# Kernel tuning notes

Measured on AMD Instinct MI355X. Metric: run time of the kernel, lower is better.

## Reference

```python
import jax, jax.numpy as jnp
import numpy as np

D = 1024
H = 16
DK = D // H


def apply_rope(x):
    # x: [B, H, T, dk]; interleaved-pair RoPE as in the torch source
    T, dim = x.shape[-2], x.shape[-1]
    inv_freq = 1.0 / (10000.0 ** (jnp.arange(0, dim, 2, dtype=x.dtype) / dim))  # [dk/2]
    pos = jnp.arange(T, dtype=x.dtype)
    sinusoid = pos[:, None] * inv_freq[None, :]  # [T, dk/2]
    sin, cos = jnp.sin(sinusoid), jnp.cos(sinusoid)
    x1, x2 = x[..., ::2], x[..., 1::2]
    rot = jnp.stack([x1 * cos - x2 * sin, x1 * sin + x2 * cos], axis=-1)
    return rot.reshape(x.shape)


def setup_inputs() -> dict:
    key = jax.random.key(0)
    k1, k2, k3, k4, k5 = jax.random.split(key, 5)
    B, T = 2, 2048
    s = 1.0 / np.sqrt(D)
    return {
        "x": jax.random.normal(k1, (B, T, D), dtype=jnp.float32),
        "W_qkv": jax.random.normal(k2, (D, 3 * D), dtype=jnp.float32) * s,
        "b_qkv": jnp.zeros((3 * D,), dtype=jnp.float32),
        "W_out": jax.random.normal(k3, (D, D), dtype=jnp.float32) * s,
        "b_out": jnp.zeros((D,), dtype=jnp.float32),
    }


def reference(x, W_qkv, b_qkv, W_out, b_out):
    B, T, C = x.shape
    qkv = x @ W_qkv + b_qkv  # [B, T, 3D]
    qkv = qkv.reshape(B, T, 3, H, DK).transpose(2, 0, 3, 1, 4)  # [3, B, H, T, dk]
    q, k, v = qkv[0], qkv[1], qkv[2]
    q, k = apply_rope(q), apply_rope(k)
    scores = jnp.einsum("bhtd,bhsd->bhts", q, k) / jnp.sqrt(jnp.asarray(DK, x.dtype))
    causal = jnp.tril(jnp.ones((T, T), dtype=bool))
    scores = jnp.where(causal, scores, jnp.asarray(-1e9, x.dtype))
    probs = jax.nn.softmax(scores, axis=-1)
    attn = jnp.einsum("bhts,bhsd->bhtd", probs, v)  # [B, H, T, dk]
    out = attn.transpose(0, 2, 1, 3).reshape(B, T, C)  # b h t d -> b t (h d)
    return out @ W_out + b_out
```

## Files before the change

### kernel.cpp

```cpp
#include <hip/hip_runtime.h>
#include <math.h>

#define DMODEL 1024
#define NHEAD  16
#define HDK    64
#define BATCH  2
#define SEQ    2048
#define MROWS  (BATCH*SEQ)
#define NQKV   (3*DMODEL)
#define LOG2_10000 13.287712379549449f
#define INV2PI 0.15915494309189535f
#define SCALE_LOG2E 0.1803368801111137f
#define M_FIX 8.0f

typedef __attribute__((ext_vector_type(8))) short bf16x8;
typedef __attribute__((ext_vector_type(4))) float f32x4;

__device__ __forceinline__ short f2bf(float f) {
    union { float f; unsigned u; } v; v.f = f;
    unsigned r = v.u + 0x7fffu + ((v.u >> 16) & 1u);
    return (short)(r >> 16);
}

__device__ __forceinline__ short bf_hi(float f) {
    union { float f; unsigned u; } v; v.f = f;
    return (short)(v.u >> 16);
}

__device__ __forceinline__ float fast_exp2(float x) {
#if __has_builtin(__builtin_amdgcn_exp2f)
    return __builtin_amdgcn_exp2f(x);
#else
    return exp2f(x);
#endif
}

__device__ __forceinline__ void gld_lds16(const short* g, short* l) {
    __builtin_amdgcn_global_load_lds(
        (const __attribute__((address_space(1))) void*)g,
        (__attribute__((address_space(3))) void*)l, 16, 0, 0);
}

__global__ __launch_bounds__(256) void prep_kernel(
    const float* __restrict__ x, const float* __restrict__ wqkv,
    const float* __restrict__ wout,
    short* __restrict__ xb, short* __restrict__ wqkv_t, short* __restrict__ wout_t)
{
    __shared__ short tile[32][33];
    const int tid = threadIdx.x;
    if (blockIdx.x < 2048) {
        const int i = (blockIdx.x * 256 + tid) * 8;
        float4 a = *(const float4*)(x + i);
        float4 b = *(const float4*)(x + i + 4);
        bf16x8 o;
        o[0] = f2bf(a.x); o[1] = f2bf(a.y); o[2] = f2bf(a.z); o[3] = f2bf(a.w);
        o[4] = f2bf(b.x); o[5] = f2bf(b.y); o[6] = f2bf(b.z); o[7] = f2bf(b.w);
        *(bf16x8*)(xb + i) = o;
        return;
    }
    const int bx = blockIdx.x - 2048;
    int nx = bx & 127;
    const int ky = bx >> 7;
    const float* in; short* out; int N;
    if (nx < 96) { in = wqkv; out = wqkv_t; N = NQKV; }
    else         { in = wout; out = wout_t; N = DMODEL; nx -= 96; }
    const int tx = tid & 31, ty = tid >> 5;
    const int n0 = nx * 32, k0 = ky * 32;
    #pragma unroll
    for (int i = 0; i < 32; i += 8)
        tile[ty + i][tx] = f2bf(in[(size_t)(k0 + ty + i) * N + n0 + tx]);
    __syncthreads();
    #pragma unroll
    for (int i = 0; i < 32; i += 8)
        out[(size_t)(n0 + ty + i) * DMODEL + k0 + tx] = tile[tx][ty + i];
}

__global__ __launch_bounds__(256) void qkv_gemm_kernel(
    const short* __restrict__ xb, const short* __restrict__ Wt,
    const float* __restrict__ bias,
    short* __restrict__ qd, short* __restrict__ kd, short* __restrict__ vtb)
{
    __shared__ __align__(16) short As[128 * 32];
    __shared__ __align__(16) short Bs[128 * 32];
    const int tid = threadIdx.x;
    const int lane = tid & 63, wave = tid >> 6;
    const int wm = wave & 1, wn = wave >> 1;
    const int l15 = lane & 15, quad = lane >> 4;
    const int n0 = blockIdx.x * 128, m0 = blockIdx.y * 128;
    const int srow = lane >> 2, sc = lane & 3;

    const short* gA1 = xb + (size_t)(m0 + wave * 32 + srow) * DMODEL + sc * 8;
    const short* gA2 = gA1 + (size_t)16 * DMODEL;
    const short* gB1 = Wt + (size_t)(n0 + wave * 32 + srow) * DMODEL + sc * 8;
    const short* gB2 = gB1 + (size_t)16 * DMODEL;
    short* lA1 = As + (wave * 32) * 32;
    short* lA2 = As + (wave * 32 + 16) * 32;
    short* lB1 = Bs + (wave * 32) * 32;
    short* lB2 = Bs + (wave * 32 + 16) * 32;

    f32x4 zero = {0.f, 0.f, 0.f, 0.f};
    f32x4 acc[4][4];
    #pragma unroll
    for (int i = 0; i < 4; ++i)
        #pragma unroll
        for (int j = 0; j < 4; ++j) acc[i][j] = zero;

    for (int k0 = 0; k0 < DMODEL; k0 += 32) {
        __syncthreads();
        gld_lds16(gA1 + k0, lA1);
        gld_lds16(gA2 + k0, lA2);
        gld_lds16(gB1 + k0, lB1);
        gld_lds16(gB2 + k0, lB2);
        __syncthreads();
        bf16x8 af[4], bfr[4];
        #pragma unroll
        for (int i = 0; i < 4; ++i)
            af[i] = *(const bf16x8*)&As[(wm * 64 + i * 16 + l15) * 32 + quad * 8];
        #pragma unroll
        for (int j = 0; j < 4; ++j)
            bfr[j] = *(const bf16x8*)&Bs[(wn * 64 + j * 16 + l15) * 32 + quad * 8];
        #pragma unroll
        for (int i = 0; i < 4; ++i)
            #pragma unroll
            for (int j = 0; j < 4; ++j)
                acc[i][j] = __builtin_amdgcn_mfma_f32_16x16x32_bf16(af[i], bfr[j], acc[i][j], 0, 0, 0);
    }

    const int which = n0 >> 10;
    float biasv[4], invf[4];
    int hh[4], dd[4];
    #pragma unroll
    for (int j = 0; j < 4; ++j) {
        const int n = n0 + wn * 64 + j * 16 + l15;
        biasv[j] = bias[n];
        hh[j] = (n & 1023) >> 6;
        dd[j] = n & 63;
        invf[j] = INV2PI * exp2f(-((float)(dd[j] & ~1) / 64.f) * LOG2_10000);
    }
    #pragma unroll
    for (int i = 0; i < 4; ++i) {
        #pragma unroll
        for (int r = 0; r < 4; ++r) {
            const int m = m0 + wm * 64 + i * 16 + quad * 4 + r;
            const int b = m >> 11, t = m & (SEQ - 1);
            #pragma unroll
            for (int j = 0; j < 4; ++j) {
                float val = acc[i][j][r] + biasv[j];
                if (which < 2) {
                    const float rev = (float)t * invf[j];
                    const float fr = rev - floorf(rev);
                    const float s = __builtin_amdgcn_sinf(fr);
                    const float c = __builtin_amdgcn_cosf(fr);
                    const float partner = __shfl_xor(val, 1);
                    val = (lane & 1) ? (partner * s + val * c) : (val * c - partner * s);
                    short* dst = (which == 0) ? qd : kd;
                    dst[((size_t)(b * NHEAD + hh[j]) * SEQ + t) * HDK + dd[j]] = f2bf(val);
                } else {
                    vtb[((size_t)(b * NHEAD + hh[j]) * HDK + dd[j]) * SEQ + t] = f2bf(val);
                }
            }
        }
    }
}

__global__ __launch_bounds__(256) void attn_mfma_kernel(
    const short* __restrict__ qd, const short* __restrict__ kd,
    const short* __restrict__ vt, short* __restrict__ od)
{
    __shared__ __align__(16) short Ks[2][2][64 * 32];
    __shared__ __align__(16) short Vs[2][2][64 * 32];
    __shared__ __align__(16) short Ps[4][16][66];
    const int tid = threadIdx.x, lane = tid & 63, w = tid >> 6;
    const int l15 = lane & 15, quad = lane >> 4;
    const int id = (int)blockIdx.x;
    const int c = id & 7, kk = id >> 3;
    const int qp = kk & 15, jj = kk >> 4;
    const int hb = c + 8 * jj;
    const int h = hb & 15, b = hb >> 4;
    const size_t base = ((size_t)(b * NHEAD + h)) * SEQ * HDK;
    const int srow = tid >> 2, sc = tid & 3;
    const int lofs = tid * 8;
    f32x4 zero = {0.f, 0.f, 0.f, 0.f};

    const int qtile[2] = { qp, 31 - qp };
    const short* kp0 = kd + base + (size_t)srow * HDK + sc * 8;
    const short* vp0 = vt + base + (size_t)srow * SEQ + sc * 8;
    const short* kp1 = kp0 + (size_t)64 * HDK;
    const short* vp1 = vp0 + 64;

    #pragma unroll 1
    for (int qi = 0; qi < 2; ++qi) {
        const int q0 = qtile[qi] * 64;
        bf16x8 qf[2];
        {
            const short* qrow = qd + base + (size_t)(q0 + w * 16 + l15) * HDK;
            qf[0] = *(const bf16x8*)(qrow + quad * 8);
            qf[1] = *(const bf16x8*)(qrow + 32 + quad * 8);
        }
        float l_acc[4] = {0.f, 0.f, 0.f, 0.f};
        f32x4 o[4];
        #pragma unroll
        for (int j = 0; j < 4; ++j) o[j] = zero;

        const int nkt = q0 / 64 + 1;
        const int npair = (nkt + 1) >> 1;

        bf16x8 rk[2][2], rv[2][2];
        rk[0][0] = *(const bf16x8*)kp0; rk[0][1] = *(const bf16x8*)(kp0 + 32);
        rv[0][0] = *(const bf16x8*)vp0; rv[0][1] = *(const bf16x8*)(vp0 + 32);
        rk[1][0] = *(const bf16x8*)kp1; rk[1][1] = *(const bf16x8*)(kp1 + 32);
        rv[1][0] = *(const bf16x8*)vp1; rv[1][1] = *(const bf16x8*)(vp1 + 32);

        for (int p = 0; p < npair; ++p) {
            __syncthreads();
            *(bf16x8*)&Ks[0][0][lofs] = rk[0][0]; *(bf16x8*)&Ks[0][1][lofs] = rk[0][1];
            *(bf16x8*)&Vs[0][0][lofs] = rv[0][0]; *(bf16x8*)&Vs[0][1][lofs] = rv[0][1];
            *(bf16x8*)&Ks[1][0][lofs] = rk[1][0]; *(bf16x8*)&Ks[1][1][lofs] = rk[1][1];
            *(bf16x8*)&Vs[1][0][lofs] = rv[1][0]; *(bf16x8*)&Vs[1][1][lofs] = rv[1][1];
            __syncthreads();
            if (p + 1 < npair) {
                const int sn = (2 * p + 2) * 64;
                const short* kn = kd + base + (size_t)(sn + srow) * HDK + sc * 8;
                const short* vn = vt + base + (size_t)srow * SEQ + sn + sc * 8;
                rk[0][0] = *(const bf16x8*)kn; rk[0][1] = *(const bf16x8*)(kn + 32);
                rv[0][0] = *(const bf16x8*)vn; rv[0][1] = *(const bf16x8*)(vn + 32);
                const short* kn2 = kn + (size_t)64 * HDK;
                const short* vn2 = vn + 64;
                rk[1][0] = *(const bf16x8*)kn2; rk[1][1] = *(const bf16x8*)(kn2 + 32);
                rv[1][0] = *(const bf16x8*)vn2; rv[1][1] = *(const bf16x8*)(vn2 + 32);
            } else if (qi == 0) {
                rk[0][0] = *(const bf16x8*)kp0; rk[0][1] = *(const bf16x8*)(kp0 + 32);
                rv[0][0] = *(const bf16x8*)vp0; rv[0][1] = *(const bf16x8*)(vp0 + 32);
                rk[1][0] = *(const bf16x8*)kp1; rk[1][1] = *(const bf16x8*)(kp1 + 32);
                rv[1][0] = *(const bf16x8*)vp1; rv[1][1] = *(const bf16x8*)(vp1 + 32);
            }

            #pragma unroll
            for (int tt = 0; tt < 2; ++tt) {
                const int kt = 2 * p + tt;
                if (tt == 1 && kt >= nkt) break;
                f32x4 sacc[4];
                #pragma unroll
                for (int j = 0; j < 4; ++j) {
                    bf16x8 kf0 = *(const bf16x8*)&Ks[tt][0][(j * 16 + l15) * 32 + quad * 8];
                    bf16x8 kf1 = *(const bf16x8*)&Ks[tt][1][(j * 16 + l15) * 32 + quad * 8];
                    sacc[j] = __builtin_amdgcn_mfma_f32_16x16x32_bf16(qf[0], kf0, zero, 0, 0, 0);
                    sacc[j] = __builtin_amdgcn_mfma_f32_16x16x32_bf16(qf[1], kf1, sacc[j], 0, 0, 0);
                }
                if (kt == nkt - 1) {
                    const int s0 = kt * 64;
                    #pragma unroll
                    for (int j = 0; j < 4; ++j) {
                        const int scol = s0 + j * 16 + l15;
                        #pragma unroll
                        for (int r = 0; r < 4; ++r) {
                            const int trow = q0 + w * 16 + quad * 4 + r;
                            const float sv = sacc[j][r] * SCALE_LOG2E - M_FIX;
                            const float pv = (scol > trow) ? 0.f : fast_exp2(sv);
                            l_acc[r] += pv;
                            Ps[w][quad * 4 + r][j * 16 + l15] = bf_hi(pv);
                        }
                    }
                } else {
                    #pragma unroll
                    for (int j = 0; j < 4; ++j)
                        #pragma unroll
                        for (int r = 0; r < 4; ++r) {
                            const float pv = fast_exp2(sacc[j][r] * SCALE_LOG2E - M_FIX);
                            l_acc[r] += pv;
                            Ps[w][quad * 4 + r][j * 16 + l15] = bf_hi(pv);
                        }
                }
                bf16x8 pf0 = *(const bf16x8*)&Ps[w][l15][quad * 8];
                bf16x8 pf1 = *(const bf16x8*)&Ps[w][l15][32 + quad * 8];
                #pragma unroll
                for (int j = 0; j < 4; ++j) {
                    bf16x8 vf0 = *(const bf16x8*)&Vs[tt][0][(j * 16 + l15) * 32 + quad * 8];
                    bf16x8 vf1 = *(const bf16x8*)&Vs[tt][1][(j * 16 + l15) * 32 + quad * 8];
                    o[j] = __builtin_amdgcn_mfma_f32_16x16x32_bf16(pf0, vf0, o[j], 0, 0, 0);
                    o[j] = __builtin_amdgcn_mfma_f32_16x16x32_bf16(pf1, vf1, o[j], 0, 0, 0);
                }
            }
        }

        #pragma unroll
        for (int r = 0; r < 4; ++r) {
            float sr = l_acc[r];
            #pragma unroll
            for (int off = 1; off < 16; off <<= 1) sr += __shfl_xor(sr, off);
            l_acc[r] = sr;
        }
        #pragma unroll
        for (int r = 0; r < 4; ++r) {
            const float inv = 1.f / l_acc[r];
            const int t = q0 + w * 16 + quad * 4 + r;
            #pragma unroll
            for (int j = 0; j < 4; ++j)
                od[((size_t)(b * SEQ + t) * NHEAD + h) * HDK + j * 16 + l15] =
                    f2bf(o[j][r] * inv);
        }
    }
}

__global__ __launch_bounds__(256) void out_gemm_kernel(
    const short* __restrict__ Ab, const short* __restrict__ Wt,
    const float* __restrict__ bias, float* __restrict__ out)
{
    __shared__ __align__(16) short As[128 * 32];
    __shared__ __align__(16) short Bs[128 * 32];
    const int tid = threadIdx.x;
    const int lane = tid & 63, wave = tid >> 6;
    const int wm = wave & 1, wn = wave >> 1;
    const int l15 = lane & 15, quad = lane >> 4;
    const int n0 = blockIdx.x * 128, m0 = blockIdx.y * 128;
    const int srow = lane >> 2, sc = lane & 3;

    const short* gA1 = Ab + (size_t)(m0 + wave * 32 + srow) * DMODEL + sc * 8;
    const short* gA2 = gA1 + (size_t)16 * DMODEL;
    const short* gB1 = Wt + (size_t)(n0 + wave * 32 + srow) * DMODEL + sc * 8;
    const short* gB2 = gB1 + (size_t)16 * DMODEL;
    short* lA1 = As + (wave * 32) * 32;
    short* lA2 = As + (wave * 32 + 16) * 32;
    short* lB1 = Bs + (wave * 32) * 32;
    short* lB2 = Bs + (wave * 32 + 16) * 32;

    f32x4 zero = {0.f, 0.f, 0.f, 0.f};
    f32x4 acc[4][4];
    #pragma unroll
    for (int i = 0; i < 4; ++i)
        #pragma unroll
        for (int j = 0; j < 4; ++j) acc[i][j] = zero;

    for (int k0 = 0; k0 < DMODEL; k0 += 32) {
        __syncthreads();
        gld_lds16(gA1 + k0, lA1);
        gld_lds16(gA2 + k0, lA2);
        gld_lds16(gB1 + k0, lB1);
        gld_lds16(gB2 + k0, lB2);
        __syncthreads();
        bf16x8 af[4], bfr[4];
        #pragma unroll
        for (int i = 0; i < 4; ++i)
            af[i] = *(const bf16x8*)&As[(wm * 64 + i * 16 + l15) * 32 + quad * 8];
        #pragma unroll
        for (int j = 0; j < 4; ++j)
            bfr[j] = *(const bf16x8*)&Bs[(wn * 64 + j * 16 + l15) * 32 + quad * 8];
        #pragma unroll
        for (int i = 0; i < 4; ++i)
            #pragma unroll
            for (int j = 0; j < 4; ++j)
                acc[i][j] = __builtin_amdgcn_mfma_f32_16x16x32_bf16(af[i], bfr[j], acc[i][j], 0, 0, 0);
    }

    #pragma unroll
    for (int j = 0; j < 4; ++j) {
        const int n = n0 + wn * 64 + j * 16 + l15;
        const float bv = bias[n];
        #pragma unroll
        for (int i = 0; i < 4; ++i)
            #pragma unroll
            for (int r = 0; r < 4; ++r) {
                const int m = m0 + wm * 64 + i * 16 + quad * 4 + r;
                out[(size_t)m * DMODEL + n] = acc[i][j][r] + bv;
            }
    }
}

extern "C" void kernel_launch(void* const* d_in, const int* in_sizes, int n_in,
                              void* d_out, int out_size, void* d_ws, size_t ws_size,
                              hipStream_t stream) {
    const float* x    = (const float*)d_in[0];
    const float* Wqkv = (const float*)d_in[1];
    const float* bqkv = (const float*)d_in[2];
    const float* Wout = (const float*)d_in[3];
    const float* bout = (const float*)d_in[4];
    float* out = (float*)d_out;

    short* ws = (short*)d_ws;
    short* xb     = ws;
    short* wqkv_t = xb + (size_t)4 * 1024 * 1024;
    short* wout_t = wqkv_t + (size_t)3 * 1024 * 1024;
    short* qd     = wout_t + (size_t)1024 * 1024;
    short* kd     = qd + (size_t)4 * 1024 * 1024;
    short* vtb    = kd + (size_t)4 * 1024 * 1024;
    short* attn   = vtb + (size_t)4 * 1024 * 1024;

    prep_kernel<<<2048 + 4096, 256, 0, stream>>>(x, Wqkv, Wout, xb, wqkv_t, wout_t);

    qkv_gemm_kernel<<<dim3(NQKV / 128, MROWS / 128), 256, 0, stream>>>(
        xb, wqkv_t, bqkv, qd, kd, vtb);

    attn_mfma_kernel<<<512, 256, 0, stream>>>(qd, kd, vtb, attn);

    out_gemm_kernel<<<dim3(DMODEL / 128, MROWS / 128), 256, 0, stream>>>(
        attn, wout_t, bout, out);
}
```

Baseline: 198.3 us.

## Process paired causal query tiles jointly, sharing each K/V tile load

Each block used to run its two query tiles (qp and 31-qp) one after the other, loading the key/value tiles twice. Now both tiles are processed in one pass over the key tiles, so every staged K/V tile feeds both query tiles while the short tile is still active. Global and LDS traffic for K/V drops and the work per barrier grows. In exchange the wave holds more live registers (two accumulator sets), K/V staging drops from two tiles per iteration to one so there are more barriers, and the extra register pressure may lower occupancy.

```diff
diff --git a/kernel.cpp b/kernel.cpp
--- a/kernel.cpp
+++ b/kernel.cpp
@@ -167,9 +167,9 @@
     const short* __restrict__ qd, const short* __restrict__ kd,
     const short* __restrict__ vt, short* __restrict__ od)
 {
-    __shared__ __align__(16) short Ks[2][2][64 * 32];
-    __shared__ __align__(16) short Vs[2][2][64 * 32];
-    __shared__ __align__(16) short Ps[4][16][66];
+    __shared__ __align__(16) short Ks[2][64 * 32];
+    __shared__ __align__(16) short Vs[2][64 * 32];
+    __shared__ __align__(16) short Ps[4][2][16][66];
     const int tid = threadIdx.x, lane = tid & 63, w = tid >> 6;
     const int l15 = lane & 15, quad = lane >> 4;
     const int id = (int)blockIdx.x;
@@ -182,122 +182,152 @@
     const int lofs = tid * 8;
     f32x4 zero = {0.f, 0.f, 0.f, 0.f};
 
-    const int qtile[2] = { qp, 31 - qp };
-    const short* kp0 = kd + base + (size_t)srow * HDK + sc * 8;
-    const short* vp0 = vt + base + (size_t)srow * SEQ + sc * 8;
-    const short* kp1 = kp0 + (size_t)64 * HDK;
-    const short* vp1 = vp0 + 64;
-
-    #pragma unroll 1
-    for (int qi = 0; qi < 2; ++qi) {
-        const int q0 = qtile[qi] * 64;
-        bf16x8 qf[2];
-        {
-            const short* qrow = qd + base + (size_t)(q0 + w * 16 + l15) * HDK;
-            qf[0] = *(const bf16x8*)(qrow + quad * 8);
-            qf[1] = *(const bf16x8*)(qrow + 32 + quad * 8);
-        }
-        float l_acc[4] = {0.f, 0.f, 0.f, 0.f};
-        f32x4 o[4];
-        #pragma unroll
-        for (int j = 0; j < 4; ++j) o[j] = zero;
-
-        const int nkt = q0 / 64 + 1;
-        const int npair = (nkt + 1) >> 1;
-
-        bf16x8 rk[2][2], rv[2][2];
-        rk[0][0] = *(const bf16x8*)kp0; rk[0][1] = *(const bf16x8*)(kp0 + 32);
-        rv[0][0] = *(const bf16x8*)vp0; rv[0][1] = *(const bf16x8*)(vp0 + 32);
-        rk[1][0] = *(const bf16x8*)kp1; rk[1][1] = *(const bf16x8*)(kp1 + 32);
-        rv[1][0] = *(const bf16x8*)vp1; rv[1][1] = *(const bf16x8*)(vp1 + 32);
-
-        for (int p = 0; p < npair; ++p) {
-            __syncthreads();
-            *(bf16x8*)&Ks[0][0][lofs] = rk[0][0]; *(bf16x8*)&Ks[0][1][lofs] = rk[0][1];
-            *(bf16x8*)&Vs[0][0][lofs] = rv[0][0]; *(bf16x8*)&Vs[0][1][lofs] = rv[0][1];
-            *(bf16x8*)&Ks[1][0][lofs] = rk[1][0]; *(bf16x8*)&Ks[1][1][lofs] = rk[1][1];
-            *(bf16x8*)&Vs[1][0][lofs] = rv[1][0]; *(bf16x8*)&Vs[1][1][lofs] = rv[1][1];
-            __syncthreads();
-            if (p + 1 < npair) {
-                const int sn = (2 * p + 2) * 64;
-                const short* kn = kd + base + (size_t)(sn + srow) * HDK + sc * 8;
-                const short* vn = vt + base + (size_t)srow * SEQ + sn + sc * 8;
-                rk[0][0] = *(const bf16x8*)kn; rk[0][1] = *(const bf16x8*)(kn + 32);
-                rv[0][0] = *(const bf16x8*)vn; rv[0][1] = *(const bf16x8*)(vn + 32);
-                const short* kn2 = kn + (size_t)64 * HDK;
-                const short* vn2 = vn + 64;
-                rk[1][0] = *(const bf16x8*)kn2; rk[1][1] = *(const bf16x8*)(kn2 + 32);
-                rv[1][0] = *(const bf16x8*)vn2; rv[1][1] = *(const bf16x8*)(vn2 + 32);
-            } else if (qi == 0) {
-                rk[0][0] = *(const bf16x8*)kp0; rk[0][1] = *(const bf16x8*)(kp0 + 32);
-                rv[0][0] = *(const bf16x8*)vp0; rv[0][1] = *(const bf16x8*)(vp0 + 32);
-                rk[1][0] = *(const bf16x8*)kp1; rk[1][1] = *(const bf16x8*)(kp1 + 32);
-                rv[1][0] = *(const bf16x8*)vp1; rv[1][1] = *(const bf16x8*)(vp1 + 32);
-            }
-
-            #pragma unroll
-            for (int tt = 0; tt < 2; ++tt) {
-                const int kt = 2 * p + tt;
-                if (tt == 1 && kt >= nkt) break;
-                f32x4 sacc[4];
+    const int q0A = qp * 64;
+    const int q0B = (31 - qp) * 64;
+    const int nktB = 32 - qp;
+
+    bf16x8 qfA[2], qfB[2];
+    {
+        const short* qrA = qd + base + (size_t)(q0A + w * 16 + l15) * HDK;
+        qfA[0] = *(const bf16x8*)(qrA + quad * 8);
+        qfA[1] = *(const bf16x8*)(qrA + 32 + quad * 8);
+        const short* qrB = qd + base + (size_t)(q0B + w * 16 + l15) * HDK;
+        qfB[0] = *(const bf16x8*)(qrB + quad * 8);
+        qfB[1] = *(const bf16x8*)(qrB + 32 + quad * 8);
+    }
+    float lA[4] = {0.f, 0.f, 0.f, 0.f}, lB[4] = {0.f, 0.f, 0.f, 0.f};
+    f32x4 oA[4], oB[4];
+    #pragma unroll
+    for (int j = 0; j < 4; ++j) { oA[j] = zero; oB[j] = zero; }
+
+    const short* kp = kd + base + (size_t)srow * HDK + sc * 8;
+    const short* vp = vt + base + (size_t)srow * SEQ + sc * 8;
+    bf16x8 rk0 = *(const bf16x8*)kp, rk1 = *(const bf16x8*)(kp + 32);
+    bf16x8 rv0 = *(const bf16x8*)vp, rv1 = *(const bf16x8*)(vp + 32);
+
+    for (int kt = 0; kt < nktB; ++kt) {
+        __syncthreads();
+        *(bf16x8*)&Ks[0][lofs] = rk0; *(bf16x8*)&Ks[1][lofs] = rk1;
+        *(bf16x8*)&Vs[0][lofs] = rv0; *(bf16x8*)&Vs[1][lofs] = rv1;
+        __syncthreads();
+        if (kt + 1 < nktB) {
+            const short* kn = kp + (size_t)(kt + 1) * 64 * HDK;
+            const short* vn = vp + (kt + 1) * 64;
+            rk0 = *(const bf16x8*)kn; rk1 = *(const bf16x8*)(kn + 32);
+            rv0 = *(const bf16x8*)vn; rv1 = *(const bf16x8*)(vn + 32);
+        }
+        const bool doA = (kt <= qp);
+
+        f32x4 sA[4], sB[4];
+        #pragma unroll
+        for (int j = 0; j < 4; ++j) {
+            bf16x8 kf0 = *(const bf16x8*)&Ks[0][(j * 16 + l15) * 32 + quad * 8];
+            bf16x8 kf1 = *(const bf16x8*)&Ks[1][(j * 16 + l15) * 32 + quad * 8];
+            sB[j] = __builtin_amdgcn_mfma_f32_16x16x32_bf16(qfB[0], kf0, zero, 0, 0, 0);
+            sB[j] = __builtin_amdgcn_mfma_f32_16x16x32_bf16(qfB[1], kf1, sB[j], 0, 0, 0);
+            if (doA) {
+                sA[j] = __builtin_amdgcn_mfma_f32_16x16x32_bf16(qfA[0], kf0, zero, 0, 0, 0);
+                sA[j] = __builtin_amdgcn_mfma_f32_16x16x32_bf16(qfA[1], kf1, sA[j], 0, 0, 0);
+            }
+        }
+
+        if (doA) {
+            if (kt == qp) {
+                const int s0 = kt * 64;
                 #pragma unroll
                 for (int j = 0; j < 4; ++j) {
-                    bf16x8 kf0 = *(const bf16x8*)&Ks[tt][0][(j * 16 + l15) * 32 + quad * 8];
-                    bf16x8 kf1 = *(const bf16x8*)&Ks[tt][1][(j * 16 + l15) * 32 + quad * 8];
-                    sacc[j] = __builtin_amdgcn_mfma_f32_16x16x32_bf16(qf[0], kf0, zero, 0, 0, 0);
-                    sacc[j] = __builtin_amdgcn_mfma_f32_16x16x32_bf16(qf[1], kf1, sacc[j], 0, 0, 0);
+                    const int scol = s0 + j * 16 + l15;
+                    #pragma unroll
+                    for (int r = 0; r < 4; ++r) {
+                        const int trow = q0A + w * 16 + quad * 4 + r;
+                        const float sv = sA[j][r] * SCALE_LOG2E - M_FIX;
+                        const float pv = (scol > trow) ? 0.f : fast_exp2(sv);
+                        lA[r] += pv;
+                        Ps[w][0][quad * 4 + r][j * 16 + l15] = bf_hi(pv);
+                    }
                 }
-                if (kt == nkt - 1) {
-                    const int s0 = kt * 64;
+            } else {
+                #pragma unroll
+                for (int j = 0; j < 4; ++j)
                     #pragma unroll
-                    for (int j = 0; j < 4; ++j) {
-                        const int scol = s0 + j * 16 + l15;
-                        #pragma unroll
-                        for (int r = 0; r < 4; ++r) {
-                            const int trow = q0 + w * 16 + quad * 4 + r;
-                            const float sv = sacc[j][r] * SCALE_LOG2E - M_FIX;
-                            const float pv = (scol > trow) ? 0.f : fast_exp2(sv);
-                            l_acc[r] += pv;
-                            Ps[w][quad * 4 + r][j * 16 + l15] = bf_hi(pv);
-                        }
+                    for (int r = 0; r < 4; ++r) {
+                        const float pv = fast_exp2(sA[j][r] * SCALE_LOG2E - M_FIX);
+                        lA[r] += pv;
+                        Ps[w][0][quad * 4 + r][j * 16 + l15] = bf_hi(pv);
                     }
-                } else {
-                    #pragma unroll
-                    for (int j = 0; j < 4; ++j)
-                        #pragma unroll
-                        for (int r = 0; r < 4; ++r) {
-                            const float pv = fast_exp2(sacc[j][r] * SCALE_LOG2E - M_FIX);
-                            l_acc[r] += pv;
-                            Ps[w][quad * 4 + r][j * 16 + l15] = bf_hi(pv);
-                        }
+            }
+        }
+        if (kt == nktB - 1) {
+            const int s0 = kt * 64;
+            #pragma unroll
+            for (int j = 0; j < 4; ++j) {
+                const int scol = s0 + j * 16 + l15;
+                #pragma unroll
+                for (int r = 0; r < 4; ++r) {
+                    const int trow = q0B + w * 16 + quad * 4 + r;
+                    const float sv = sB[j][r] * SCALE_LOG2E - M_FIX;
+                    const float pv = (scol > trow) ? 0.f : fast_exp2(sv);
+                    lB[r] += pv;
+                    Ps[w][1][quad * 4 + r][j * 16 + l15] = bf_hi(pv);
                 }
-                bf16x8 pf0 = *(const bf16x8*)&Ps[w][l15][quad * 8];
-                bf16x8 pf1 = *(const bf16x8*)&Ps[w][l15][32 + quad * 8];
+            }
+        } else {
+            #pragma unroll
+            for (int j = 0; j < 4; ++j)
                 #pragma unroll
-                for (int j = 0; j < 4; ++j) {
-                    bf16x8 vf0 = *(const bf16x8*)&Vs[tt][0][(j * 16 + l15) * 32 + quad * 8];
-                    bf16x8 vf1 = *(const bf16x8*)&Vs[tt][1][(j * 16 + l15) * 32 + quad * 8];
-                    o[j] = __builtin_amdgcn_mfma_f32_16x16x32_bf16(pf0, vf0, o[j], 0, 0, 0);
-                    o[j] = __builtin_amdgcn_mfma_f32_16x16x32_bf16(pf1, vf1, o[j], 0, 0, 0);
+                for (int r = 0; r < 4; ++r) {
+                    const float pv = fast_exp2(sB[j][r] * SCALE_LOG2E - M_FIX);
+                    lB[r] += pv;
+                    Ps[w][1][quad * 4 + r][j * 16 + l15] = bf_hi(pv);
                 }
-            }
-        }
-
-        #pragma unroll
-        for (int r = 0; r < 4; ++r) {
-            float sr = l_acc[r];
-            #pragma unroll
-            for (int off = 1; off < 16; off <<= 1) sr += __shfl_xor(sr, off);
-            l_acc[r] = sr;
-        }
-        #pragma unroll
-        for (int r = 0; r < 4; ++r) {
-            const float inv = 1.f / l_acc[r];
-            const int t = q0 + w * 16 + quad * 4 + r;
-            #pragma unroll
-            for (int j = 0; j < 4; ++j)
-                od[((size_t)(b * SEQ + t) * NHEAD + h) * HDK + j * 16 + l15] =
-                    f2bf(o[j][r] * inv);
+        }
+
+        if (doA) {
+            bf16x8 pf0 = *(const bf16x8*)&Ps[w][0][l15][quad * 8];
+            bf16x8 pf1 = *(const bf16x8*)&Ps[w][0][l15][32 + quad * 8];
+            #pragma unroll
+            for (int j = 0; j < 4; ++j) {
+                bf16x8 vf0 = *(const bf16x8*)&Vs[0][(j * 16 + l15) * 32 + quad * 8];
+                bf16x8 vf1 = *(const bf16x8*)&Vs[1][(j * 16 + l15) * 32 + quad * 8];
+                oA[j] = __builtin_amdgcn_mfma_f32_16x16x32_bf16(pf0, vf0, oA[j], 0, 0, 0);
+                oA[j] = __builtin_amdgcn_mfma_f32_16x16x32_bf16(pf1, vf1, oA[j], 0, 0, 0);
+            }
+        }
+        {
+            bf16x8 pf0 = *(const bf16x8*)&Ps[w][1][l15][quad * 8];
+            bf16x8 pf1 = *(const bf16x8*)&Ps[w][1][l15][32 + quad * 8];
+            #pragma unroll
+            for (int j = 0; j < 4; ++j) {
+                bf16x8 vf0 = *(const bf16x8*)&Vs[0][(j * 16 + l15) * 32 + quad * 8];
+                bf16x8 vf1 = *(const bf16x8*)&Vs[1][(j * 16 + l15) * 32 + quad * 8];
+                oB[j] = __builtin_amdgcn_mfma_f32_16x16x32_bf16(pf0, vf0, oB[j], 0, 0, 0);
+                oB[j] = __builtin_amdgcn_mfma_f32_16x16x32_bf16(pf1, vf1, oB[j], 0, 0, 0);
+            }
+        }
+    }
+
+    #pragma unroll
+    for (int r = 0; r < 4; ++r) {
+        float sa = lA[r], sb = lB[r];
+        #pragma unroll
+        for (int off = 1; off < 16; off <<= 1) {
+            sa += __shfl_xor(sa, off);
+            sb += __shfl_xor(sb, off);
+        }
+        lA[r] = sa; lB[r] = sb;
+    }
+    #pragma unroll
+    for (int r = 0; r < 4; ++r) {
+        const float invA = 1.f / lA[r];
+        const float invB = 1.f / lB[r];
+        const int tA = q0A + w * 16 + quad * 4 + r;
+        const int tB = q0B + w * 16 + quad * 4 + r;
+        #pragma unroll
+        for (int j = 0; j < 4; ++j) {
+            od[((size_t)(b * SEQ + tA) * NHEAD + h) * HDK + j * 16 + l15] =
+                f2bf(oA[j][r] * invA);
+            od[((size_t)(b * SEQ + tB) * NHEAD + h) * HDK + j * 16 + l15] =
+                f2bf(oB[j][r] * invB);
         }
     }
 }
```

Result: no change. 201.0 us (+1.3%).
